# Kernel optimization log

Measured on AMD Instinct MI355X. Metric: run time of the kernel, lower is better.

## Reference

```python
import jax, jax.numpy as jnp
import numpy as np

T = 1 << 20  # hash-table size for bilateral-grid vertices
PRIMES = jnp.array([73856093, 19349663, 83492791, 49979687, 24036583], dtype=jnp.int32)
RGB2YUV = jnp.array([[0.299, 0.587, 0.114], [-0.168736, -0.331264, 0.5], [0.5, -0.418688, -0.081312]], dtype=jnp.float32)
YUV_OFF = jnp.array([0.0, 128.0, 128.0], dtype=jnp.float32)
SIG = jnp.array([8.0, 2.0, 2.0], dtype=jnp.float32)  # sigma_luma, sigma_chroma, sigma_chroma (mode=0)
SIGMA_SPATIAL = 7.0
LAM = 200.0
A_DIAG_MIN = 1e-5
CG_MAXITER = 12
BISTO_ITERS = 10
EPS = 1e-12
DIM = 5


def _hash(c):  # (..., 5) int32 -> flat bin id in [0, T)
    return (c * PRIMES).sum(-1) & (T - 1)


def _norm_max(x):
    s = jnp.clip(jnp.max(x, axis=(1, 2, 3), keepdims=True), 1e-5, 1.0)
    return x / s


def _conv(x, w, b, stride, pad):
    y = jax.lax.conv_general_dilated(x, w, (stride, stride), ((pad, pad), (pad, pad)), dimension_numbers=('NCHW', 'OIHW', 'NCHW'))
    return y + b[None, :, None, None]


def _gn(x, g, b, groups=2, eps=1e-5):
    B, C, H, W = x.shape
    xg = x.reshape(B, groups, -1)
    mu = xg.mean(-1, keepdims=True)
    var = xg.var(-1, keepdims=True)
    xg = (xg - mu) * jax.lax.rsqrt(var + eps)
    return xg.reshape(B, C, H, W) * g[None, :, None, None] + b[None, :, None, None]


def _reppad(x):
    return jnp.pad(x, ((0, 0), (0, 0), (1, 1), (1, 1)), mode='edge')


def _resize(x, h, w):
    B, C = x.shape[:2]
    return jax.image.resize(x, (B, C, h, w), method='linear')


def _bilateral_solve(guide_hwc, target_hwc, conf_hw):
    # fast bilateral solver (Barron & Poole): splat -> bistochastize -> PCG on grid -> slice
    H, W, C = target_hwc.shape
    N = H * W
    yuv = guide_hwc.reshape(N, 3) @ RGB2YUV.T + YUV_OFF
    yy, xx = jnp.meshgrid(jnp.arange(H, dtype=jnp.float32), jnp.arange(W, dtype=jnp.float32), indexing='ij')
    sp = jnp.stack([xx, yy], -1).reshape(N, 2) / SIGMA_SPATIAL
    coords = jnp.concatenate([jnp.floor(sp), jnp.floor(yuv / SIG)], -1).astype(jnp.int32)  # (N,5)
    h = _hash(coords)
    occ = jnp.zeros((T,), bool).at[h].set(True)
    ctab = jnp.full((T, 5), -1, jnp.int32).at[h].set(coords)
    # precompute 1-2-1 blur neighbor gathers along each of the 5 grid dims
    nhs, vals = [], []
    for d in range(DIM):
        for off in (-1, 1):
            nc = ctab.at[:, d].add(off)
            nh = _hash(nc)
            nhs.append(nh)
            vals.append(occ & occ[nh] & jnp.all(ctab[nh] == nc, axis=-1))
    occf = occ[:, None]

    def blur(v):  # (T,k)
        out = (2.0 * DIM) * v
        for nh, va in zip(nhs, vals):
            out = out + jnp.where(va[:, None], v[nh], 0.0)
        return jnp.where(occf, out, 0.0)

    def splat(v):  # (N,k) -> (T,k)
        return jax.ops.segment_sum(v, h, num_segments=T)

    # bistochastization
    m = splat(jnp.ones((N, 1), jnp.float32))
    n = occf.astype(jnp.float32)
    for _ in range(BISTO_ITERS):
        n = jnp.sqrt(n * m / (blur(n) + EPS))
    m = n * blur(n)

    w = conf_hw.reshape(N, 1)
    w_splat = splat(w)
    b = splat(w * target_hwc.reshape(N, C))
    y0 = b / (w_splat + EPS)
    A_diag = jnp.maximum(LAM * (m - (2.0 * DIM) * n * n) + w_splat, A_DIAG_MIN)
    Minv = 1.0 / A_diag

    def A(v):  # A = lam*(Dm - Dn B Dn) + diag(splat(w))
        return LAM * (m * v - n * blur(n * v)) + w_splat * v

    x0 = y0
    r0 = b - A(x0)
    z0 = Minv * r0

    def step(st, _):
        x, r, z, p = st
        Ap = A(p)
        rz = (r * z).sum(0)
        alpha = rz / ((p * Ap).sum(0) + EPS)
        x = x + alpha * p
        r = r - alpha * Ap
        z = Minv * r
        beta = (r * z).sum(0) / (rz + EPS)
        p = z + beta * p
        return (x, r, z, p), None

    (x, _, _, _), _ = jax.lax.scan(step, (x0, r0, z0, z0), None, length=CG_MAXITER)
    return x[h].reshape(H, W, C)  # slice


def _forward(image, feature, pred, w1, b1, g1, be1, w2, b2, g2, be2, wd1, bd1, gd1, bed1, wd2, bd2, gd2, bed2, wf, bf):
    image = _norm_max(image)
    feature = _norm_max(feature)
    inp = jax.lax.stop_gradient(jnp.concatenate([image, pred], axis=1))
    x1 = jax.nn.relu(_gn(_conv(_reppad(inp), w1, b1, 2, 0), g1, be1))
    x2 = jax.nn.relu(_gn(_conv(_reppad(x1), w2, b2, 2, 0), g2, be2))
    dx1 = jax.nn.relu(_gn(_conv(x2, wd1, bd1, 1, 1), gd1, bed1))
    dx1 = _resize(dx1, x1.shape[2], x1.shape[3])
    dx2 = jax.nn.relu(_gn(_conv(jnp.concatenate([dx1, x1], 1), wd2, bd2, 1, 1), gd2, bed2))
    dx2 = _resize(dx2, inp.shape[2], inp.shape[3])
    conf = 0.5 * (jnp.tanh(_conv(_reppad(dx2), wf, bf, 1, 0)) + 1.0)
    conf = conf / jnp.maximum(conf.max(), 1e-5)
    guide = jax.lax.stop_gradient(feature) * 255.0
    out = jax.vmap(_bilateral_solve)(guide.transpose(0, 2, 3, 1), pred.transpose(0, 2, 3, 1), conf[:, 0])
    return out.transpose(0, 3, 1, 2), conf


def setup_inputs():
    key = jax.random.key(0)
    ks = jax.random.split(key, 8)
    B, H, W = 2, 384, 512

    def cw(k, shape, fan_in):
        return jax.random.normal(k, shape, jnp.float32) * (1.0 / np.sqrt(fan_in))

    return {
        'image': jax.random.uniform(ks[0], (B, 3, H, W), jnp.float32),
        'feature': jax.random.uniform(ks[1], (B, 3, H, W), jnp.float32),
        'pred': jax.random.uniform(ks[2], (B, 3, H, W), jnp.float32),
        'w1': cw(ks[3], (16, 6, 4, 4), 6 * 16), 'b1': jnp.zeros((16,), jnp.float32),
        'g1': jnp.ones((16,), jnp.float32), 'be1': jnp.zeros((16,), jnp.float32),
        'w2': cw(ks[4], (16, 16, 4, 4), 16 * 16), 'b2': jnp.zeros((16,), jnp.float32),
        'g2': jnp.ones((16,), jnp.float32), 'be2': jnp.zeros((16,), jnp.float32),
        'wd1': cw(ks[5], (16, 16, 3, 3), 16 * 9), 'bd1': jnp.zeros((16,), jnp.float32),
        'gd1': jnp.ones((16,), jnp.float32), 'bed1': jnp.zeros((16,), jnp.float32),
        'wd2': cw(ks[6], (16, 32, 3, 3), 32 * 9), 'bd2': jnp.zeros((16,), jnp.float32),
        'gd2': jnp.ones((16,), jnp.float32), 'bed2': jnp.zeros((16,), jnp.float32),
        'wf': cw(ks[7], (1, 16, 3, 3), 16 * 9), 'bf': jnp.zeros((1,), jnp.float32),
    }


def reference(image, feature, pred, w1, b1, g1, be1, w2, b2, g2, be2, wd1, bd1, gd1, bed1, wd2, bd2, gd2, bed2, wf, bf):
    return _forward(image, feature, pred, w1, b1, g1, be1, w2, b2, g2, be2, wd1, bd1, gd1, bed1, wd2, bd2, gd2, bed2, wf, bf)
```

## Files before the change

### kernel.cpp

```cpp
#include <hip/hip_runtime.h>

#define H_ 384
#define W_ 512
#define N_ (H_*W_)
#define B_ 2
#define T_ 1048576
#define TMASK_ 0xFFFFFu
#define G2N_ ((2*N_)/256)
#define G2T_ ((2*T_)/256)
#define CHS_ 64
#define RZ0_ 192
#define RZB_ 2688
#define PAP0_ 5568
#define PAPB_ 2496
#define GN0_ 10560

__device__ __forceinline__ int prime(int d){
  switch(d){
    case 0: return 73856093;
    case 1: return 19349663;
    case 2: return 83492791;
    case 3: return 49979687;
    default: return 24036583;
  }
}

__device__ __forceinline__ float clampScale(float s){ return fminf(fmaxf(s,1e-5f),1.0f); }

__device__ __forceinline__ double blockReduceD(double v){
  __shared__ double sh[4];
  for(int s=32;s>0;s>>=1) v += __shfl_down(v,s,64);
  int lane=threadIdx.x&63, w=threadIdx.x>>6;
  if(lane==0) sh[w]=v;
  __syncthreads();
  double r = sh[0]+sh[1]+sh[2]+sh[3];
  __syncthreads();
  return r;
}
__device__ __forceinline__ float blockReduceMaxF(float v){
  __shared__ float sh[4];
  for(int s=32;s>0;s>>=1) v = fmaxf(v,__shfl_down(v,s,64));
  int lane=threadIdx.x&63, w=threadIdx.x>>6;
  if(lane==0) sh[w]=v;
  __syncthreads();
  float r = fmaxf(fmaxf(sh[0],sh[1]),fmaxf(sh[2],sh[3]));
  __syncthreads();
  return r;
}

__device__ __forceinline__ void redAdd(double* base, int c, double v){
  atomicAdd(&base[c*CHS_ + ((blockIdx.x&7)<<3)], v);
}
__device__ __forceinline__ float redSum(const double* base, int c){
  double s=0.0;
  #pragma unroll
  for(int j=0;j<8;j++) s += base[c*CHS_ + j*8];
  return (float)s;
}

__device__ __forceinline__ void gnStats(const double* acc, int b, int c, double len,
                                        float* mf, float* rs){
  const double* ba = acc + (b*2 + (c>>3))*128;
  double s=0.0,s2=0.0;
  #pragma unroll
  for(int j=0;j<8;j++){ s+=ba[j*8]; s2+=ba[64+j*8]; }
  double mean = s/len;
  double var = s2/len - mean*mean;
  *rs = (float)(1.0/sqrt(var + 1e-5));
  *mf = (float)mean;
}


__global__ __launch_bounds__(256) void k_maxes(const float4* img4, const float4* feat4, float* scal){
  const int PB = (3*N_)/4;
  for(int b=0;b<2;b++){
    float lm=0.f, lf=0.f;
    for(int idx = blockIdx.x*256+threadIdx.x; idx<PB; idx += gridDim.x*256){
      float4 a=img4[(size_t)b*PB+idx], c=feat4[(size_t)b*PB+idx];
      lm=fmaxf(lm, fmaxf(fmaxf(a.x,a.y),fmaxf(a.z,a.w)));
      lf=fmaxf(lf, fmaxf(fmaxf(c.x,c.y),fmaxf(c.z,c.w)));
    }
    lm=blockReduceMaxF(lm); lf=blockReduceMaxF(lf);
    if(threadIdx.x==0){
      atomicMax((int*)&scal[b],   __float_as_int(lm));
      atomicMax((int*)&scal[2+b], __float_as_int(lf));
    }
  }
}

template<int PLANE4>
__global__ __launch_bounds__(256) void k_gnrelu(const float4* in, float4* out, const double* acc,
                                                const float* gamma, const float* beta){
  int idx = blockIdx.x*256 + threadIdx.x;
  int t = idx / PLANE4;
  int c = t & 15, b = t >> 4;
  __shared__ float smf, srs, sg, sbe;
  if(threadIdx.x==0){
    float mf, rs;
    gnStats(acc, b, c, 8.0*(double)(PLANE4*4), &mf, &rs);
    smf=mf; srs=rs; sg=gamma[c]; sbe=beta[c];
  }
  __syncthreads();
  float mf=smf, rs=srs, g=sg, be=sbe;
  float4 v = in[idx];
  v.x = fmaxf((v.x-mf)*rs*g+be, 0.f);
  v.y = fmaxf((v.y-mf)*rs*g+be, 0.f);
  v.z = fmaxf((v.z-mf)*rs*g+be, 0.f);
  v.w = fmaxf((v.w-mf)*rs*g+be, 0.f);
  out[idx] = v;
}

template<bool SCALEA,int NCH,int K,int S,bool EDGE,int IH,int IW,int NOC>
__device__ __forceinline__ void conv_accum(const float* __restrict__ plane0, int icBase, float sA,
                                           int oy, int ox, const float* wlds, float acc[NOC]){
  for(int ic=0; ic<NCH; ic++){
    const float* plane = plane0 + (size_t)ic*IH*IW;
    #pragma unroll
    for(int ky=0;ky<K;ky++){
      int iy = oy*S + ky - 1;
      int cy = min(max(iy,0),IH-1);
      bool yin = (iy>=0)&&(iy<IH);
      const float* row = plane + cy*IW;
      #pragma unroll
      for(int kx=0;kx<K;kx++){
        int ix = ox*S + kx - 1;
        float v;
        if(EDGE){
          int cx = min(max(ix,0),IW-1);
          v = row[cx];
          if(SCALEA) v = v / sA;
        } else {
          bool inb = yin && ix>=0 && ix<IW;
          if(inb){
            v = row[ix];
            if(SCALEA) v = v / sA;
          } else v = 0.f;
        }
        const float* wp = &wlds[((icBase+ic)*K*K + ky*K + kx)*NOC];
        #pragma unroll
        for(int q=0;q<NOC;q++) acc[q] += v*wp[q];
      }
    }
  }
}

template<bool SCALEA,int ICA,int ICB,int K,int S,bool EDGE,int IH,int IW,int OH,int OW,int OCSPLIT>
__global__ __launch_bounds__(256) void k_convT(const float* __restrict__ inA, const float* __restrict__ inB,
                        const float* __restrict__ wt, const float* __restrict__ bias,
                        float* __restrict__ out, double* gnaccOut, const float* scal){
  constexpr int IC = ICA+ICB;
  constexpr int NOC = 16/OCSPLIT;
  constexpr int PB = (B_*OH*OW)/256;
  __shared__ float wlds[IC*K*K*NOC];
  __shared__ float blds[NOC];
  int pb  = blockIdx.x % PB;
  int ocg = blockIdx.x / PB;
  int ocBase = ocg*NOC;
  for(int i=threadIdx.x; i<IC*K*K*NOC; i+=256){
    int q = i % NOC, ickk = i / NOC;
    wlds[i] = wt[(ocBase+q)*IC*K*K + ickk];
  }
  if(threadIdx.x<NOC) blds[threadIdx.x]=bias[ocBase+threadIdx.x];
  __syncthreads();
  int idx = pb*256+threadIdx.x;
  int ox = idx % OW; int t=idx/OW; int oy=t%OH; int b=t/OH;
  float sA = SCALEA ? clampScale(scal[b]) : 1.0f;
  float acc[NOC];
  #pragma unroll
  for(int q=0;q<NOC;q++) acc[q]=0.f;
  conv_accum<SCALEA,ICA,K,S,EDGE,IH,IW,NOC>(inA + (size_t)b*ICA*IH*IW, 0, sA, oy, ox, wlds, acc);
  if constexpr(ICB>0)
    conv_accum<false,(ICB>0?ICB:1),K,S,EDGE,IH,IW,NOC>(inB + (size_t)b*ICB*IH*IW, ICA, 1.0f, oy, ox, wlds, acc);
  double s=0.0,s2=0.0;
  #pragma unroll
  for(int q=0;q<NOC;q++){
    float vv = acc[q] + blds[q];
    out[(((size_t)b*16+(ocBase+q))*OH+oy)*OW+ox] = vv;
    s += vv; s2 += (double)vv*(double)vv;
  }
  s=blockReduceD(s); s2=blockReduceD(s2);
  if(threadIdx.x==0){
    int grp = ocBase>>3;
    int sub = (blockIdx.x&7)<<3;
    atomicAdd(&gnaccOut[(b*2+grp)*128 + sub],      s);
    atomicAdd(&gnaccOut[(b*2+grp)*128 + 64 + sub], s2);
  }
}

template<int IH,int IW>
__global__ __launch_bounds__(256) void k_resize2x(const float* __restrict__ in, float* __restrict__ out,
                                                  const double* acc, const float* gamma, const float* beta){
  constexpr int QP = IH*IW;
  constexpr int OW = 2*IW;
  int idx = blockIdx.x*256 + threadIdx.x;
  int q = idx % QP; int t = idx / QP;
  int qx = q % IW, qy = q / IW;
  int c = t & 15, b = t >> 4;
  __shared__ float smf, srs, sg, sbe;
  if(threadIdx.x==0){
    float mf, rs;
    gnStats(acc, b, c, 8.0*(double)QP, &mf, &rs);
    smf=mf; srs=rs; sg=gamma[c]; sbe=beta[c];
  }
  __syncthreads();
  float mf=smf, rs=srs, g=sg, be=sbe;
  const float* plane = in + (size_t)t*QP;
  int ym = max(qy-1,0), yp = min(qy+1,IH-1);
  int xm = max(qx-1,0), xp = min(qx+1,IW-1);
  const float* r0 = plane + ym*IW;
  const float* r1 = plane + qy*IW;
// ... 10 lines not shown
  *(float2*)po        = rE;
  *(float2*)(po + OW) = rO;
}

__global__ __launch_bounds__(256) void k_conv5(const float* in, const float* wf, const float* bf,
                                               float* confr, float* scal){
  int idx = blockIdx.x*256 + threadIdx.x;
  int ph = idx % (N_/2); int b = idx / (N_/2);
  int oyh = ph / W_, ox = ph % W_;
  int oy0 = oyh*2;
  float acc0 = bf[0], acc1 = bf[0];
  for(int ic=0; ic<16; ic++){
    const float* plane = in + ((size_t)b*16+ic)*N_;
    #pragma unroll
    for(int ky=0;ky<3;ky++){
      int iy0 = min(max(oy0+ky-1,0),H_-1);
      int iy1 = min(max(oy0+ky,0),H_-1);
      const float* row0 = plane + iy0*W_;
      const float* row1 = plane + iy1*W_;
      #pragma unroll
      for(int kx=0;kx<3;kx++){
        int ix = min(max(ox+kx-1,0),W_-1);
        float w = wf[(ic*3+ky)*3+kx];
        acc0 += row0[ix]*w;
        acc1 += row1[ix]*w;
      }
    }
  }
  float c0 = 0.5f*(tanhf(acc0)+1.0f);
  float c1 = 0.5f*(tanhf(acc1)+1.0f);
  confr[(size_t)b*N_ + oy0*W_ + ox]     = c0;
  confr[(size_t)b*N_ + (oy0+1)*W_ + ox] = c1;
  float mx = blockReduceMaxF(fmaxf(c0,c1));
  if(threadIdx.x==0) atomicMax((int*)&scal[4], __float_as_int(mx));
}


__global__ __launch_bounds__(256) void k_px1(const float* feat, const float* scal,
                                             int* hpix, int2* cpix2, int* winner){
  int idx = blockIdx.x*256 + threadIdx.x;
  int b = idx / N_, pix = idx % N_;
  int y = pix / W_, x = pix % W_;
  float sF = clampScale(scal[2+b]);
  const float* fb = feat + (size_t)b*3*N_;
  float R  = __fmul_rn(__fdiv_rn(fb[pix],      sF), 255.0f);
  float G  = __fmul_rn(__fdiv_rn(fb[N_+pix],   sF), 255.0f);
  float Bl = __fmul_rn(__fdiv_rn(fb[2*N_+pix], sF), 255.0f);
  float Y = __fadd_rn(__fadd_rn(__fadd_rn(__fmul_rn(0.299f,R),     __fmul_rn(0.587f,G)),  __fmul_rn(0.114f,Bl)), 0.0f);
  float U = __fadd_rn(__fadd_rn(__fadd_rn(__fmul_rn(-0.168736f,R), __fmul_rn(-0.331264f,G)), __fmul_rn(0.5f,Bl)), 128.0f);
  float V = __fadd_rn(__fadd_rn(__fadd_rn(__fmul_rn(0.5f,R),       __fmul_rn(-0.418688f,G)), __fmul_rn(-0.081312f,Bl)), 128.0f);
  int c[5];
  c[0] = (int)floorf(__fdiv_rn((float)x, 7.0f));
  c[1] = (int)floorf(__fdiv_rn((float)y, 7.0f));
  c[2] = (int)floorf(__fdiv_rn(Y, 8.0f));
  c[3] = (int)floorf(__fdiv_rn(U, 2.0f));
  c[4] = (int)floorf(__fdiv_rn(V, 2.0f));
  unsigned hh = 0;
  #pragma unroll
  for(int d=0;d<5;d++) hh += (unsigned)c[d]*(unsigned)prime(d);
  hh &= TMASK_;
  hpix[idx]=(int)hh;
  cpix2[idx]=make_int2(c[0] | (c[1]<<10) | (c[2]<<20), c[3] | (c[4]<<10));
  atomicMax(&winner[(size_t)b*T_+(int)hh], pix);
}


__global__ __launch_bounds__(256) void k_cnt(const int* winner, int* bcnt){
  int t = blockIdx.x*256 + threadIdx.x;
  bool occ = winner[t] >= 0;
  __shared__ int wc[4];
  unsigned long long mk = __ballot(occ);
  int lane = threadIdx.x & 63, w = threadIdx.x >> 6;
  if(lane==0) wc[w] = __popcll(mk);
  __syncthreads();
  if(threadIdx.x==0) bcnt[blockIdx.x] = wc[0]+wc[1]+wc[2]+wc[3];
}

__global__ __launch_bounds__(256) void k_scan(const int* bcnt, int* boff, int* count){
  __shared__ int sh[256];
  __shared__ int carry;
  if(threadIdx.x==0) carry=0;
  __syncthreads();
  for(int chunk=0; chunk<32; ++chunk){
    if(chunk==16){
      if(threadIdx.x==0){ count[0]=carry; carry=0; }
      __syncthreads();
    }
    int v = bcnt[chunk*256+threadIdx.x];
    sh[threadIdx.x]=v;
    __syncthreads();
    for(int s2=1;s2<256;s2<<=1){
      int add = (threadIdx.x>=s2)? sh[threadIdx.x-s2] : 0;
      __syncthreads();
      sh[threadIdx.x]+=add;
      __syncthreads();
    }
    int incl = sh[threadIdx.x];
    boff[chunk*256+threadIdx.x] = carry + incl - v;
    __syncthreads();
    if(threadIdx.x==255) carry += incl;
    __syncthreads();
  }
  if(threadIdx.x==0) count[1]=carry;
}

__global__ __launch_bounds__(256) void k_cmp(const int* winner, const int* boff,
                                             int2* cidx2, int* slot_of){
  int t = blockIdx.x*256 + threadIdx.x;
  int b = t / T_;
  int wn = winner[t];
  bool occ = wn >= 0;
  __shared__ int wc[4];
  unsigned long long mk = __ballot(occ);
  int lane = threadIdx.x & 63, w = threadIdx.x >> 6;
  if(lane==0) wc[w] = __popcll(mk);
  __syncthreads();
  int wpre = 0;
  for(int k2=0;k2<4;k2++) if(k2<w) wpre += wc[k2];
  if(occ){
    int li = boff[blockIdx.x] + wpre + __popcll(mk & ((1ull<<lane)-1ull));
    int gi = b*N_ + li;
    cidx2[t] = make_int2(gi, wn);
    slot_of[gi] = t - b*T_;
  }
}

__global__ __launch_bounds__(256) void k_px3(int* hpix_gpix, const int2* cidx2, const float* confr,
                                             const float* scal, float* confout, const float* pred,
                                             float* mcomp, float4* splat4, float* mcompE, float* splatE){
  int idx = blockIdx.x*256 + threadIdx.x;
  int b = idx / N_, pix = idx % N_;
  int2 cw = cidx2[(size_t)b*T_ + hpix_gpix[idx]];
  int gi = cw.x;
  hpix_gpix[idx] = gi;
  float w = confr[idx] / fmaxf(scal[4], 1e-5f);
  confout[idx] = w;
  const float* pb = pred + (size_t)b*3*N_;
  float v0 = __fmul_rn(w, pb[pix]);
  float v1 = __fmul_rn(w, pb[N_+pix]);
  float v2 = __fmul_rn(w, pb[2*N_+pix]);
  if(cw.y == pix){
    splat4[gi] = make_float4(v0,v1,v2,w);
    mcomp[gi] = 1.0f;
  } else {
    float* s = splatE + 4*(size_t)gi;
    atomicAdd(s+0, v0);
    atomicAdd(s+1, v1);
    atomicAdd(s+2, v2);
    atomicAdd(s+3, w);
    atomicAdd(&mcompE[gi], 1.0f);
  }
}

__global__ __launch_bounds__(256) void k_bisto0(const int* count, const int* slot_of,
                      const int2* cpix2, const int2* cidx2, int* nbr,
                      float* mcomp, const float* mcompE, float4* splat4, const float4* splatE4,
                      float* nd){
  int i = blockIdx.x*256 + threadIdx.x;
  int b = i / N_, li = i - b*N_;
  if(li >= count[b]) return;
  int hh = slot_of[i];
  const int2* c2b = cidx2 + (size_t)b*T_;
  int2 cself = c2b[hh];
  int2 cp = cpix2[(size_t)b*N_ + cself.y];
  float4 sp = splat4[i]; float4 se = splatE4[i];
  sp.x+=se.x; sp.y+=se.y; sp.z+=se.z; sp.w+=se.w;
  splat4[i]=sp;
  float mTot = mcomp[i] + mcompE[i];
  mcomp[i]=mTot;
  float bv = 10.f;
  #pragma unroll
  for(int j=0;j<10;j++){
    int d=j>>1; int off=(j&1)?1:-1;
    unsigned nh = ((unsigned)hh + (unsigned)(off*prime(d))) & TMASK_;
    int nb = -1;
    int2 cn2 = c2b[nh];
    if(cn2.y>=0){
      int2 cn = cpix2[(size_t)b*N_ + cn2.y];
      int e0 = cp.x + (d==0?off: d==1?off*(1<<10) : d==2?off*(1<<20) : 0);
      int e1 = cp.y + (d==3?off: d==4?off*(1<<10) : 0);
      if(cn.x==e0 && cn.y==e1) nb = cn2.x;
    }
    nbr[(size_t)j*(2*N_)+i]=nb;
    if(nb>=0) bv += 1.0f;
  }
  nd[i] = sqrtf(1.0f*mTot/(bv+1e-12f));
}

__global__ __launch_bounds__(256) void k_bisto(const int* count, const int* nbr,
                                               const float* ns, float* nd, const float* mc){
  int i = blockIdx.x*256 + threadIdx.x;
  int b = i / N_, li = i - b*N_;
  if(li >= count[b]) return;
  float nv = ns[i];
  float bv = 10.f*nv;
  #pragma unroll
  for(int j=0;j<10;j++){
    int nb = nbr[(size_t)j*(2*N_)+i];
    if(nb>=0) bv += ns[nb];
  }
  nd[i] = sqrtf(nv*mc[i]/(bv+1e-12f));
}

__global__ __launch_bounds__(256) void k_Ar0(const int* count, const int* nbr, const float* n,
                      const float4* splat4, float4* meta4, float4* x4, float4* r4, float4* p4,
                      double* rz0){
  int i = blockIdx.x*256 + threadIdx.x;
  int b = i / N_, li = i - b*N_;
  double a0=0.0,a1=0.0,a2=0.0;
  if(li < count[b]){
    float4 vb4 = splat4[i];
    float wsi = vb4.w;
    float nv = n[i];
    float x0 = vb4.x/(wsi+1e-12f);
    float x1 = vb4.y/(wsi+1e-12f);
    float x2 = vb4.z/(wsi+1e-12f);
    float bv = 10.f*nv;
    float s0=10.f*(nv*x0), s1=10.f*(nv*x1), s2=10.f*(nv*x2);
    #pragma unroll
    for(int j=0;j<10;j++){
      int nb = nbr[(size_t)j*(2*N_)+i];
      if(nb>=0){
        float4 vbn = splat4[nb];
        float nn = n[nb];
        bv += nn;
        s0 += nn*(vbn.x/(vbn.w+1e-12f));
        s1 += nn*(vbn.y/(vbn.w+1e-12f));
        s2 += nn*(vbn.z/(vbn.w+1e-12f));
      }
    }
    float mfin = nv*bv;
    float Ad = fmaxf(200.0f*(mfin - 10.f*nv*nv) + wsi, 1e-5f);
    float mi = 1.0f/Ad;
    float A0 = 200.f*(mfin*x0 - nv*s0) + wsi*x0;
    float A1 = 200.f*(mfin*x1 - nv*s1) + wsi*x1;
    float A2 = 200.f*(mfin*x2 - nv*s2) + wsi*x2;
    float r0v = vb4.x-A0, r1v = vb4.y-A1, r2v = vb4.z-A2;
    float z0=mi*r0v, z1=mi*r1v, z2=mi*r2v;
    meta4[i]=make_float4(nv,mfin,wsi,mi);
    x4[i]=make_float4(x0,x1,x2,0.f);
    r4[i]=make_float4(r0v,r1v,r2v,mi);
    p4[i]=make_float4(z0,z1,z2,nv);
    a0=(double)r0v*z0; a1=(double)r1v*z1; a2=(double)r2v*z2;
  }
  a0=blockReduceD(a0); a1=blockReduceD(a1); a2=blockReduceD(a2);
  if(threadIdx.x==0){
    double* base = rz0 + b*RZB_;
    redAdd(base,0,a0); redAdd(base,1,a1); redAdd(base,2,a2);
  }
}

__global__ __launch_bounds__(256) void k_Ap(const int* count, const int* nbr, const float4* meta4,
                     const float4* r4, const float4* pOld4, float4* pNew4, float4* Ap4,
                     const double* bNum, const double* bDen, int bstr, double* pAp){
  int i = blockIdx.x*256 + threadIdx.x;
  int b = i / N_, li = i - b*N_;
  double a0=0.0,a1=0.0,a2=0.0;
  const double* nB_ = bNum + b*bstr;
  const double* dB_ = bDen + b*bstr;
  float be0 = redSum(nB_,0) / (redSum(dB_,0)+1e-12f);
  float be1 = redSum(nB_,1) / (redSum(dB_,1)+1e-12f);
  float be2 = redSum(nB_,2) / (redSum(dB_,2)+1e-12f);
  if(li < count[b]){
    float4 mt = meta4[i];
    float nv = mt.x, mfin = mt.y, wsi = mt.z;
    float4 rs = r4[i];
    float4 ps = pOld4[i];
    float p0 = rs.w*rs.x + be0*ps.x;
    float p1 = rs.w*rs.y + be1*ps.y;
    float p2 = rs.w*rs.z + be2*ps.z;
    float s0=10.f*(nv*p0), s1=10.f*(nv*p1), s2=10.f*(nv*p2);
    #pragma unroll
    for(int j=0;j<10;j++){
      int nb = nbr[(size_t)j*(2*N_)+i];
      if(nb>=0){
        float4 rn = r4[nb];
        float4 pn = pOld4[nb];
        float nn = pn.w;
        s0 += nn*(rn.w*rn.x + be0*pn.x);
        s1 += nn*(rn.w*rn.y + be1*pn.y);
        s2 += nn*(rn.w*rn.z + be2*pn.z);
      }
    }
    float A0 = 200.f*(mfin*p0 - nv*s0) + wsi*p0;
    float A1 = 200.f*(mfin*p1 - nv*s1) + wsi*p1;
    float A2 = 200.f*(mfin*p2 - nv*s2) + wsi*p2;
    pNew4[i]=make_float4(p0,p1,p2,nv);
    Ap4[i]=make_float4(A0,A1,A2,0.f);
    a0=(double)p0*A0; a1=(double)p1*A1; a2=(double)p2*A2;
  }
  a0=blockReduceD(a0); a1=blockReduceD(a1); a2=blockReduceD(a2);
  if(threadIdx.x==0){
    double* base = pAp + b*PAPB_;
    redAdd(base,0,a0); redAdd(base,1,a1); redAdd(base,2,a2);
  }
}

__global__ __launch_bounds__(256) void k_upd1(const int* count, float4* x4, float4* r4,
                       const float4* p4, const float4* Ap4,
                       const double* rzCur, const double* pApC, double* rzNew, int doRz){
  int i = blockIdx.x*256 + threadIdx.x;
  int b = i / N_, li = i - b*N_;
  double a0=0.0,a1=0.0,a2=0.0;
  const double* rc = rzCur + b*RZB_;
  const double* pc = pApC  + b*PAPB_;
  float al0 = redSum(rc,0) / (redSum(pc,0)+1e-12f);
  float al1 = redSum(rc,1) / (redSum(pc,1)+1e-12f);
  float al2 = redSum(rc,2) / (redSum(pc,2)+1e-12f);
  if(li < count[b]){
    float4 xv = x4[i];
    float4 rv = r4[i];
    float4 pv = p4[i];
    float4 av = Ap4[i];
    float mi = rv.w;
    float x0=xv.x+al0*pv.x, x1=xv.y+al1*pv.y, x2=xv.z+al2*pv.z;
    float r0v=rv.x-al0*av.x, r1v=rv.y-al1*av.y, r2v=rv.z-al2*av.z;
    float z0=mi*r0v, z1=mi*r1v, z2=mi*r2v;
    x4[i]=make_float4(x0,x1,x2,0.f);
    r4[i]=make_float4(r0v,r1v,r2v,mi);
    a0=(double)r0v*z0; a1=(double)r1v*z1; a2=(double)r2v*z2;
  }
  if(doRz){
    a0=blockReduceD(a0); a1=blockReduceD(a1); a2=blockReduceD(a2);
    if(threadIdx.x==0){
      double* base = rzNew + b*RZB_;
      redAdd(base,0,a0); redAdd(base,1,a1); redAdd(base,2,a2);
    }
  }
}

__global__ __launch_bounds__(256) void k_out(const float4* x4, const int* gpix, float* out){
  int idx = blockIdx.x*256 + threadIdx.x;
  int b = idx / N_, pix = idx % N_;
  float4 xv = x4[gpix[idx]];
  out[((size_t)(b*3+0))*N_+pix] = xv.x;
  out[((size_t)(b*3+1))*N_+pix] = xv.y;
  out[((size_t)(b*3+2))*N_+pix] = xv.z;
}


extern "C" void kernel_launch(void* const* d_in, const int* in_sizes, int n_in,
                              void* d_out, int out_size, void* d_ws, size_t ws_size,
                              hipStream_t stream){
  const float* image=(const float*)d_in[0];
  const float* feature=(const float*)d_in[1];
  const float* pred=(const float*)d_in[2];
  const float* w1=(const float*)d_in[3];  const float* b1=(const float*)d_in[4];
  const float* g1=(const float*)d_in[5];  const float* be1=(const float*)d_in[6];
  const float* w2=(const float*)d_in[7];  const float* b2=(const float*)d_in[8];
  const float* g2=(const float*)d_in[9];  const float* be2=(const float*)d_in[10];
  const float* wd1=(const float*)d_in[11];const float* bd1=(const float*)d_in[12];
  const float* gd1=(const float*)d_in[13];const float* bed1=(const float*)d_in[14];
  const float* wd2=(const float*)d_in[15];const float* bd2=(const float*)d_in[16];
  const float* gd2=(const float*)d_in[17];const float* bed2=(const float*)d_in[18];
  const float* wf=(const float*)d_in[19]; const float* bf=(const float*)d_in[20];
  float* outp=(float*)d_out;
  float* confout = outp + (size_t)B_*3*N_;

  char* wsb=(char*)d_ws;
  float* scal=(float*)wsb;
  int* count=(int*)(wsb+256);
  double* scalD=(double*)(wsb+4096);
  double* zeroD = scalD;
  auto rzArr  = [&](int it)->double*{ return scalD + RZ0_  + it*192; };
  auto pApArr = [&](int it)->double*{ return scalD + PAP0_ + it*192; };
  auto gnAcc  = [&](int L)->double*{ return scalD + GN0_ + L*512; };

  size_t off = 131072;
  auto alloc=[&](size_t bytes)->char*{ char* pp=wsb+off; off=(off+bytes+255)&~(size_t)255; return pp; };
  const size_t ALLOC0 = off;

  float* x1   =(float*)alloc((size_t)B_*16*192*256*4);
  float* x1n  =(float*)alloc((size_t)B_*16*192*256*4);
  float* x2   =(float*)alloc((size_t)B_*16*96*128*4);
  float* x2n  =(float*)alloc((size_t)B_*16*96*128*4);
  float* dx1  =(float*)alloc((size_t)B_*16*96*128*4);
  float* dx1r =(float*)alloc((size_t)B_*16*192*256*4);
  float* dx2  =(float*)alloc((size_t)B_*16*192*256*4);
  float* dx2r =(float*)alloc((size_t)B_*16*N_*4);

  off = ALLOC0;
  int*    winner =(int*)   alloc((size_t)2*T_*4);
  int2*   cidx2  =(int2*)  alloc((size_t)2*T_*8);
  int*    hpix   =(int*)   alloc((size_t)2*N_*4);
  int2*   cpix2  =(int2*)  alloc((size_t)2*N_*8);
  int*    slot_of=(int*)   alloc((size_t)2*N_*4);
  int*    nbr    =(int*)   alloc((size_t)2*N_*10*4);
  float*  mcomp  =(float*) alloc((size_t)2*N_*4);
  float4* splat4 =(float4*)alloc((size_t)2*N_*16);
  float*  mcompE =(float*) alloc((size_t)2*N_*4);
  float*  splatE =(float*) alloc((size_t)2*N_*16);
  float*  nA     =(float*) alloc((size_t)2*N_*4);
  float*  nB     =(float*) alloc((size_t)2*N_*4);
  float4* meta4  =(float4*)alloc((size_t)2*N_*16);
  float4* x4     =(float4*)alloc((size_t)2*N_*16);
  float4* r4     =(float4*)alloc((size_t)2*N_*16);
  float4* pA4    =(float4*)alloc((size_t)2*N_*16);
  float4* pB4    =(float4*)alloc((size_t)2*N_*16);
  int*    bcnt   =(int*)   alloc((size_t)G2T_*4);
  int*    boff   =(int*)   alloc((size_t)G2T_*4);
  float4* Ap4    = splat4;
  float*  confr  = (float*)pB4;

  dim3 blk(256);

  hipMemsetAsync(wsb, 0, 4096 + 12608*8, stream);

  k_maxes<<<128,blk,0,stream>>>((const float4*)image,(const float4*)feature,scal);

  k_convT<true,3,3,4,2,true,384,512,192,256,2><<<2*((B_*192*256)/256),blk,0,stream>>>(
      image,pred,w1,b1,x1,gnAcc(0),scal);
  k_gnrelu<12288><<<(B_*16*12288)/256,blk,0,stream>>>((const float4*)x1,(float4*)x1n,gnAcc(0),g1,be1);
  k_convT<false,16,0,4,2,true,192,256,96,128,8><<<8*((B_*96*128)/256),blk,0,stream>>>(
      x1n,x1n,w2,b2,x2,gnAcc(1),scal);
  k_gnrelu<3072><<<(B_*16*3072)/256,blk,0,stream>>>((const float4*)x2,(float4*)x2n,gnAcc(1),g2,be2);
  k_convT<false,16,0,3,1,false,96,128,96,128,8><<<8*((B_*96*128)/256),blk,0,stream>>>(
      x2n,x2n,wd1,bd1,dx1,gnAcc(2),scal);
  k_resize2x<96,128><<<(B_*16*96*128)/256,blk,0,stream>>>(dx1, dx1r, gnAcc(2), gd1, bed1);
  k_convT<false,16,16,3,1,false,192,256,192,256,2><<<2*((B_*192*256)/256),blk,0,stream>>>(
      dx1r,x1n,wd2,bd2,dx2,gnAcc(3),scal);
  k_resize2x<192,256><<<(B_*16*192*256)/256,blk,0,stream>>>(dx2, dx2r, gnAcc(3), gd2, bed2);

  k_conv5<<<(B_*(N_/2))/256,blk,0,stream>>>(dx2r, wf, bf, confr, scal);

  hipMemsetAsync(winner, 0xFF, (size_t)2*T_*4, stream);
  hipMemsetAsync(cidx2,  0xFF, (size_t)2*T_*8, stream);
  hipMemsetAsync(mcomp,  0,    (size_t)2*N_*40, stream);
  k_px1<<<G2N_,blk,0,stream>>>(feature,scal,hpix,cpix2,winner);
  k_cnt<<<G2T_,blk,0,stream>>>(winner,bcnt);
  k_scan<<<1,blk,0,stream>>>(bcnt,boff,count);
  k_cmp<<<G2T_,blk,0,stream>>>(winner,boff,cidx2,slot_of);
  k_px3<<<G2N_,blk,0,stream>>>(hpix,cidx2,confr,scal,confout,pred,mcomp,splat4,mcompE,splatE);

  k_bisto0<<<G2N_,blk,0,stream>>>(count,slot_of,cpix2,cidx2,nbr,mcomp,mcompE,splat4,(const float4*)splatE,nA);
  for(int it=1; it<10; ++it){
    float* src = (it&1) ? nA : nB;
    float* dst = (it&1) ? nB : nA;
    k_bisto<<<G2N_,blk,0,stream>>>(count,nbr,src,dst,mcomp);
  }
  float* nfin = nB;

  k_Ar0<<<G2N_,blk,0,stream>>>(count,nbr,nfin,splat4,meta4,x4,r4,pA4,rzArr(0));

  float4* pbuf[2]={pA4,pB4};
  for(int it=0; it<12; ++it){
    const double* bN = (it==0) ? zeroD : rzArr(it);
    const double* bD = (it==0) ? zeroD : rzArr(it-1);
    int bstr = (it==0) ? 0 : RZB_;
    k_Ap<<<G2N_,blk,0,stream>>>(count,nbr,meta4,r4,pbuf[it&1],pbuf[(it+1)&1],Ap4,bN,bD,bstr,pApArr(it));
    k_upd1<<<G2N_,blk,0,stream>>>(count,x4,r4,pbuf[(it+1)&1],Ap4,rzArr(it),pApArr(it),rzArr(it+1),(it<11)?1:0);
  }
  k_out<<<G2N_,blk,0,stream>>>(x4,hpix,outp);

  (void)in_sizes; (void)n_in; (void)out_size; (void)ws_size;
}
```

Before: 771.9 us.

## Fuse bistochastization and PCG solver into one persistent cooperative kernel

```diff
diff --git a/kernel.cpp b/kernel.cpp
--- a/kernel.cpp
+++ b/kernel.cpp
@@ -1,4 +1,7 @@
 #include <hip/hip_runtime.h>
+#include <hip/hip_cooperative_groups.h>
+
+namespace cg = cooperative_groups;
 
 #define H_ 384
 #define W_ 512
@@ -56,6 +59,13 @@
   #pragma unroll
   for(int j=0;j<8;j++) s += base[c*CHS_ + j*8];
   return (float)s;
+}
+__device__ __forceinline__ double redSumAtomic(const double* base, int c){
+  double s=0.0;
+  #pragma unroll
+  for(int j=0;j<8;j++)
+    s += __hip_atomic_load(&base[c*CHS_ + j*8], __ATOMIC_RELAXED, __HIP_MEMORY_SCOPE_AGENT);
+  return s;
 }
 
 __device__ __forceinline__ void gnStats(const double* acc, int b, int c, double len,
@@ -372,6 +382,301 @@
   }
 }
 
+template<int K>
+__global__ __launch_bounds__(256, (K==1?3:2)) void k_solver(
+    const int* __restrict__ count, const int* __restrict__ slot_of,
+    const int2* __restrict__ cpix2, const int2* __restrict__ cidx2,
+    int* __restrict__ nbr, const float* __restrict__ mcomp,
+    const float* __restrict__ mcompE, float4* __restrict__ splat4,
+    const float4* __restrict__ splatE4, float* __restrict__ nA,
+    float* __restrict__ nB, float4* __restrict__ r4,
+    float4* __restrict__ pA4, float4* __restrict__ pB4,
+    float4* __restrict__ x4, double* __restrict__ scalD,
+    const int* __restrict__ gpix, float* __restrict__ outp){
+  constexpr int STRIDE = N_/K;
+  cg::grid_group gg = cg::this_grid();
+  int tid = blockIdx.x*256 + threadIdx.x;
+  int cnt0 = count[0], cnt1 = count[1];
+  bool lv_[2][K];
+  float mt_[2][K], nv_[2][K];
+  #pragma unroll
+  for(int e=0;e<2;e++)
+    #pragma unroll
+    for(int k=0;k<K;k++)
+      lv_[e][k] = (tid + k*STRIDE) < (e ? cnt1 : cnt0);
+
+  #pragma unroll
+  for(int e=0;e<2;e++){
+    #pragma unroll
+    for(int k=0;k<K;k++){
+      if(lv_[e][k]){
+        int i = tid + k*STRIDE + e*N_;
+        int hh = slot_of[i];
+        const int2* c2b = cidx2 + (size_t)e*T_;
+        int2 cself = c2b[hh];
+        int2 cp = cpix2[(size_t)e*N_ + cself.y];
+        float4 sp = splat4[i]; float4 se = splatE4[i];
+        sp.x+=se.x; sp.y+=se.y; sp.z+=se.z; sp.w+=se.w;
+        splat4[i]=sp;
+        float mTot = mcomp[i] + mcompE[i];
+        mt_[e][k]=mTot;
+        float bv = 10.f;
+        #pragma unroll
+        for(int j=0;j<10;j++){
+          int d=j>>1; int off=(j&1)?1:-1;
+          unsigned nh = ((unsigned)hh + (unsigned)(off*prime(d))) & TMASK_;
+          int nb = -1;
+          int2 cn2 = c2b[nh];
+          if(cn2.y>=0){
+            int2 cn = cpix2[(size_t)e*N_ + cn2.y];
+            int e0 = cp.x + (d==0?off: d==1?off*(1<<10) : d==2?off*(1<<20) : 0);
+            int e1 = cp.y + (d==3?off: d==4?off*(1<<10) : 0);
+            if(cn.x==e0 && cn.y==e1) nb = cn2.x;
+          }
+          nbr[(size_t)j*(2*N_)+i]=nb;
+          if(nb>=0) bv += 1.0f;
+        }
+        float nd0 = sqrtf(1.0f*mTot/(bv+1e-12f));
+        nv_[e][k]=nd0;
+        nA[i]=nd0;
+      }
+    }
+  }
+  gg.sync();
+
+  const float* nsrc = nA; float* ndst = nB;
+  for(int it=1; it<10; ++it){
+    #pragma unroll
+    for(int e=0;e<2;e++){
+      #pragma unroll
+      for(int k=0;k<K;k++){
+        if(lv_[e][k]){
+          int i = tid + k*STRIDE + e*N_;
+          float nvs = nv_[e][k];
+          float bv = 10.f*nvs;
+          #pragma unroll
+          for(int j=0;j<10;j++){
+            int nb = nbr[(size_t)j*(2*N_)+i];
+            if(nb>=0) bv += nsrc[nb];
+          }
+          float nn = sqrtf(nvs*mt_[e][k]/(bv+1e-12f));
+          nv_[e][k]=nn;
+          ndst[i]=nn;
+        }
+      }
+    }
+    gg.sync();
+    float* ts = (float*)nsrc; nsrc = ndst; ndst = ts;
+  }
+
+  float xx_[2][K][3], rr_[2][K][3], pp_[2][K][3], Ap_[2][K][3];
+  float mi_[2][K], mfin_[2][K], wsi_[2][K];
+  {
+    double acc[2][3] = {{0.0,0.0,0.0},{0.0,0.0,0.0}};
+    #pragma unroll
+    for(int e=0;e<2;e++){
+      #pragma unroll
+      for(int k=0;k<K;k++){
+        if(lv_[e][k]){
+          int i = tid + k*STRIDE + e*N_;
+          float4 vb4 = splat4[i];
+          float wsi = vb4.w;
+          float nv = nv_[e][k];
+          float x0 = vb4.x/(wsi+1e-12f);
+          float x1 = vb4.y/(wsi+1e-12f);
+          float x2 = vb4.z/(wsi+1e-12f);
+          float bv = 10.f*nv;
+          float s0=10.f*(nv*x0), s1=10.f*(nv*x1), s2=10.f*(nv*x2);
+          #pragma unroll
+          for(int j=0;j<10;j++){
+            int nb = nbr[(size_t)j*(2*N_)+i];
+            if(nb>=0){
+              float4 vbn = splat4[nb];
+              float nn = nsrc[nb];
+              bv += nn;
+              s0 += nn*(vbn.x/(vbn.w+1e-12f));
+              s1 += nn*(vbn.y/(vbn.w+1e-12f));
+              s2 += nn*(vbn.z/(vbn.w+1e-12f));
+            }
+          }
+          float mfin = nv*bv;
+          float Ad = fmaxf(200.0f*(mfin - 10.f*nv*nv) + wsi, 1e-5f);
+          float mi = 1.0f/Ad;
+          float A0 = 200.f*(mfin*x0 - nv*s0) + wsi*x0;
+          float A1 = 200.f*(mfin*x1 - nv*s1) + wsi*x1;
+          float A2 = 200.f*(mfin*x2 - nv*s2) + wsi*x2;
+          float r0v = vb4.x-A0, r1v = vb4.y-A1, r2v = vb4.z-A2;
+          float z0=mi*r0v, z1=mi*r1v, z2=mi*r2v;
+          r4[i]=make_float4(r0v,r1v,r2v,mi);
+          pA4[i]=make_float4(z0,z1,z2,nv);
+          xx_[e][k][0]=x0; xx_[e][k][1]=x1; xx_[e][k][2]=x2;
+          rr_[e][k][0]=r0v; rr_[e][k][1]=r1v; rr_[e][k][2]=r2v;
+          pp_[e][k][0]=z0; pp_[e][k][1]=z1; pp_[e][k][2]=z2;
+          mi_[e][k]=mi; mfin_[e][k]=mfin; wsi_[e][k]=wsi;
+          acc[e][0]+=(double)r0v*z0; acc[e][1]+=(double)r1v*z1; acc[e][2]+=(double)r2v*z2;
+        }
+      }
+    }
+    #pragma unroll
+    for(int e=0;e<2;e++){
+      #pragma unroll
+      for(int c=0;c<3;c++){
+        double r = blockReduceD(acc[e][c]);
+        if(threadIdx.x==0)
+          atomicAdd(&scalD[RZ0_ + e*RZB_ + c*CHS_ + ((blockIdx.x&7)<<3)], r);
+      }
+    }
+  }
+  gg.sync();
+
+  for(int it=0; it<12; ++it){
+    __shared__ float sbe[2][3];
+    if(threadIdx.x==0){
+      #pragma unroll
+      for(int b=0;b<2;b++){
+        if(it==0){ sbe[b][0]=0.f; sbe[b][1]=0.f; sbe[b][2]=0.f; }
+        else{
+          const double* nB_ = scalD + RZ0_ + it*192     + b*RZB_;
+          const double* dB_ = scalD + RZ0_ + (it-1)*192 + b*RZB_;
+          #pragma unroll
+          for(int c=0;c<3;c++){
+            float num = (float)redSumAtomic(nB_,c);
+            float den = (float)redSumAtomic(dB_,c);
+            sbe[b][c] = num / (den + 1e-12f);
+          }
+        }
+      }
+    }
+    __syncthreads();
+    const float4* pOld = (it&1)? pB4 : pA4;
+    float4*       pNew = (it&1)? pA4 : pB4;
+    double acc[2][3] = {{0.0,0.0,0.0},{0.0,0.0,0.0}};
+    #pragma unroll
+    for(int e=0;e<2;e++){
+      #pragma unroll
+      for(int k=0;k<K;k++){
+        if(lv_[e][k]){
+          int i = tid + k*STRIDE + e*N_;
+          float be0=sbe[e][0], be1=sbe[e][1], be2=sbe[e][2];
+          float mi=mi_[e][k], mfin=mfin_[e][k], wsi=wsi_[e][k];
+          float nvv = nv_[e][k];
+          float p0 = mi*rr_[e][k][0] + be0*pp_[e][k][0];
+          float p1 = mi*rr_[e][k][1] + be1*pp_[e][k][1];
+          float p2 = mi*rr_[e][k][2] + be2*pp_[e][k][2];
+          float s0=10.f*(nvv*p0), s1=10.f*(nvv*p1), s2=10.f*(nvv*p2);
+          #pragma unroll
+          for(int j=0;j<10;j++){
+            int nb = nbr[(size_t)j*(2*N_)+i];
+            if(nb>=0){
+              float4 rn = r4[nb];
+              float4 pn = pOld[nb];
+              float nn = pn.w;
+              s0 += nn*(rn.w*rn.x + be0*pn.x);
+              s1 += nn*(rn.w*rn.y + be1*pn.y);
+              s2 += nn*(rn.w*rn.z + be2*pn.z);
+            }
+          }
+          float A0 = 200.f*(mfin*p0 - nvv*s0) + wsi*p0;
+          float A1 = 200.f*(mfin*p1 - nvv*s1) + wsi*p1;
+          float A2 = 200.f*(mfin*p2 - nvv*s2) + wsi*p2;
+          pNew[i]=make_float4(p0,p1,p2,nvv);
+          pp_[e][k][0]=p0; pp_[e][k][1]=p1; pp_[e][k][2]=p2;
+          Ap_[e][k][0]=A0; Ap_[e][k][1]=A1; Ap_[e][k][2]=A2;
+          acc[e][0]+=(double)p0*A0; acc[e][1]+=(double)p1*A1; acc[e][2]+=(double)p2*A2;
+        }
+      }
+    }
+    #pragma unroll
+    for(int e=0;e<2;e++){
+      #pragma unroll
+      for(int c=0;c<3;c++){
+        double r = blockReduceD(acc[e][c]);
+        if(threadIdx.x==0)
+          atomicAdd(&scalD[PAP0_ + it*192 + e*PAPB_ + c*CHS_ + ((blockIdx.x&7)<<3)], r);
+      }
+    }
+    gg.sync();
+
+    __shared__ float sal[2][3];
+    if(threadIdx.x==0){
+      #pragma unroll
+      for(int b=0;b<2;b++){
+        const double* rc = scalD + RZ0_  + it*192 + b*RZB_;
+        const double* pc = scalD + PAP0_ + it*192 + b*PAPB_;
+        #pragma unroll
+        for(int c=0;c<3;c++){
+          float num = (float)redSumAtomic(rc,c);
+          float den = (float)redSumAtomic(pc,c);
+          sal[b][c] = num / (den + 1e-12f);
+        }
+      }
+    }
+    __syncthreads();
+    double bacc[2][3] = {{0.0,0.0,0.0},{0.0,0.0,0.0}};
+    #pragma unroll
+    for(int e=0;e<2;e++){
+      #pragma unroll
+      for(int k=0;k<K;k++){
+        if(lv_[e][k]){
+          int i = tid + k*STRIDE + e*N_;
+          float al0=sal[e][0], al1=sal[e][1], al2=sal[e][2];
+          xx_[e][k][0] += al0*pp_[e][k][0];
+          xx_[e][k][1] += al1*pp_[e][k][1];
+          xx_[e][k][2] += al2*pp_[e][k][2];
+          if(it<11){
+            float r0v = rr_[e][k][0] - al0*Ap_[e][k][0];
+            float r1v = rr_[e][k][1] - al1*Ap_[e][k][1];
+            float r2v = rr_[e][k][2] - al2*Ap_[e][k][2];
+            rr_[e][k][0]=r0v; rr_[e][k][1]=r1v; rr_[e][k][2]=r2v;
+            float mi = mi_[e][k];
+            r4[i]=make_float4(r0v,r1v,r2v,mi);
+            bacc[e][0]+=(double)r0v*(mi*r0v);
+            bacc[e][1]+=(double)r1v*(mi*r1v);
+            bacc[e][2]+=(double)r2v*(mi*r2v);
+          }
+        }
+      }
+    }
+    if(it<11){
+      #pragma unroll
+      for(int e=0;e<2;e++){
+        #pragma unroll
+        for(int c=0;c<3;c++){
+          double r = blockReduceD(bacc[e][c]);
+          if(threadIdx.x==0)
+            atomicAdd(&scalD[RZ0_ + (it+1)*192 + e*RZB_ + c*CHS_ + ((blockIdx.x&7)<<3)], r);
+        }
+      }
+    }
+    gg.sync();
+  }
+
+  #pragma unroll
+  for(int e=0;e<2;e++){
+    #pragma unroll
+    for(int k=0;k<K;k++){
+      if(lv_[e][k]){
+        int i = tid + k*STRIDE + e*N_;
+        x4[i]=make_float4(xx_[e][k][0],xx_[e][k][1],xx_[e][k][2],0.f);
+      }
+    }
+  }
+  gg.sync();
+  #pragma unroll
+  for(int e=0;e<2;e++){
+    #pragma unroll
+    for(int k=0;k<K;k++){
+      int pix = tid + k*STRIDE;
+      int i = pix + e*N_;
+      float4 xv = x4[gpix[i]];
+      outp[((size_t)(e*3+0))*N_+pix] = xv.x;
+      outp[((size_t)(e*3+1))*N_+pix] = xv.y;
+      outp[((size_t)(e*3+2))*N_+pix] = xv.z;
+    }
+  }
+}
+
+
 __global__ __launch_bounds__(256) void k_bisto0(const int* count, const int* slot_of,
                       const int2* cpix2, const int2* cidx2, int* nbr,
                       float* mcomp, const float* mcompE, float4* splat4, const float4* splatE4,
@@ -652,25 +957,55 @@
   k_cmp<<<G2T_,blk,0,stream>>>(winner,boff,cidx2,slot_of);
   k_px3<<<G2N_,blk,0,stream>>>(hpix,cidx2,confr,scal,confout,pred,mcomp,splat4,mcompE,splatE);
 
-  k_bisto0<<<G2N_,blk,0,stream>>>(count,slot_of,cpix2,cidx2,nbr,mcomp,mcompE,splat4,(const float4*)splatE,nA);
-  for(int it=1; it<10; ++it){
-    float* src = (it&1) ? nA : nB;
-    float* dst = (it&1) ? nB : nA;
-    k_bisto<<<G2N_,blk,0,stream>>>(count,nbr,src,dst,mcomp);
-  }
-  float* nfin = nB;
-
-  k_Ar0<<<G2N_,blk,0,stream>>>(count,nbr,nfin,splat4,meta4,x4,r4,pA4,rzArr(0));
-
-  float4* pbuf[2]={pA4,pB4};
-  for(int it=0; it<12; ++it){
-    const double* bN = (it==0) ? zeroD : rzArr(it);
-    const double* bD = (it==0) ? zeroD : rzArr(it-1);
-    int bstr = (it==0) ? 0 : RZB_;
-    k_Ap<<<G2N_,blk,0,stream>>>(count,nbr,meta4,r4,pbuf[it&1],pbuf[(it+1)&1],Ap4,bN,bD,bstr,pApArr(it));
-    k_upd1<<<G2N_,blk,0,stream>>>(count,x4,r4,pbuf[(it+1)&1],Ap4,rzArr(it),pApArr(it),rzArr(it+1),(it<11)?1:0);
-  }
-  k_out<<<G2N_,blk,0,stream>>>(x4,hpix,outp);
+  bool done = false;
+  {
+    const int* countc = count;
+    const int* slotc  = slot_of;
+    const int2* cpix2c = cpix2;
+    const int2* cidx2c = cidx2;
+    const float* mcompc = mcomp;
+    const float* mcompEc = mcompE;
+    const float4* splatE4c = (const float4*)splatE;
+    const int* gpixc = hpix;
+    void* kargs[] = {
+      (void*)&countc, (void*)&slotc, (void*)&cpix2c, (void*)&cidx2c,
+      (void*)&nbr, (void*)&mcompc, (void*)&mcompEc, (void*)&splat4,
+      (void*)&splatE4c, (void*)&nA, (void*)&nB, (void*)&r4,
+      (void*)&pA4, (void*)&pB4, (void*)&x4, (void*)&scalD,
+      (void*)&gpixc, (void*)&outp };
+    int occ1=0, occ2=0;
+    hipOccupancyMaxActiveBlocksPerMultiprocessor(&occ1,
+        reinterpret_cast<const void*>(&k_solver<1>), 256, 0);
+    hipOccupancyMaxActiveBlocksPerMultiprocessor(&occ2,
+        reinterpret_cast<const void*>(&k_solver<2>), 256, 0);
+    if(occ1 >= 3){
+      done = (hipSuccess == hipLaunchCooperativeKernel(
+          reinterpret_cast<const void*>(&k_solver<1>), dim3(N_/256), blk, kargs, 0, stream));
+    }
+    if(!done && occ2 >= 2){
+      done = (hipSuccess == hipLaunchCooperativeKernel(
+          reinterpret_cast<const void*>(&k_solver<2>), dim3(N_/512), blk, kargs, 0, stream));
+    }
+  }
+  if(!done){
+    k_bisto0<<<G2N_,blk,0,stream>>>(count,slot_of,cpix2,cidx2,nbr,mcomp,mcompE,splat4,(const float4*)splatE,nA);
+    for(int it=1; it<10; ++it){
+      float* src = (it&1) ? nA : nB;
+      float* dst = (it&1) ? nB : nA;
+      k_bisto<<<G2N_,blk,0,stream>>>(count,nbr,src,dst,mcomp);
+    }
+    float* nfin = nB;
+    k_Ar0<<<G2N_,blk,0,stream>>>(count,nbr,nfin,splat4,meta4,x4,r4,pA4,rzArr(0));
+    float4* pbuf[2]={pA4,pB4};
+    for(int it=0; it<12; ++it){
+      const double* bN = (it==0) ? zeroD : rzArr(it);
+      const double* bD = (it==0) ? zeroD : rzArr(it-1);
+      int bstr = (it==0) ? 0 : RZB_;
+      k_Ap<<<G2N_,blk,0,stream>>>(count,nbr,meta4,r4,pbuf[it&1],pbuf[(it+1)&1],Ap4,bN,bD,bstr,pApArr(it));
+      k_upd1<<<G2N_,blk,0,stream>>>(count,x4,r4,pbuf[(it+1)&1],Ap4,rzArr(it),pApArr(it),rzArr(it+1),(it<11)?1:0);
+    }
+    k_out<<<G2N_,blk,0,stream>>>(x4,hpix,outp);
+  }
 
   (void)in_sizes; (void)n_in; (void)out_size; (void)ws_size;
 }
```

After: 773.9 us. No clear change (+0.3%).

## Interleave preconditioned residual and direction in one CG buffer, hoist scalar reductions

Applied to the files above, without the earlier changes.

```diff
diff --git a/kernel.cpp b/kernel.cpp
--- a/kernel.cpp
+++ b/kernel.cpp
@@ -372,6 +372,7 @@
   }
 }
 
+
 __global__ __launch_bounds__(256) void k_bisto0(const int* count, const int* slot_of,
                       const int2* cpix2, const int2* cidx2, int* nbr,
                       float* mcomp, const float* mcompE, float4* splat4, const float4* splatE4,
@@ -423,7 +424,7 @@
 }
 
 __global__ __launch_bounds__(256) void k_Ar0(const int* count, const int* nbr, const float* n,
-                      const float4* splat4, float4* meta4, float4* x4, float4* r4, float4* p4,
+                      const float4* splat4, float4* meta4, float4* x4, float4* rS, float4* zp0,
                       double* rz0){
   int i = blockIdx.x*256 + threadIdx.x;
   int b = i / N_, li = i - b*N_;
@@ -459,8 +460,9 @@
     float z0=mi*r0v, z1=mi*r1v, z2=mi*r2v;
     meta4[i]=make_float4(nv,mfin,wsi,mi);
     x4[i]=make_float4(x0,x1,x2,0.f);
-    r4[i]=make_float4(r0v,r1v,r2v,mi);
-    p4[i]=make_float4(z0,z1,z2,nv);
+    rS[i]=make_float4(r0v,r1v,r2v,mi);
+    zp0[2*(size_t)i]   = make_float4(z0,z1,z2,mi);
+    zp0[2*(size_t)i+1] = make_float4(z0,z1,z2,nv);
     a0=(double)r0v*z0; a1=(double)r1v*z1; a2=(double)r2v*z2;
   }
   a0=blockReduceD(a0); a1=blockReduceD(a1); a2=blockReduceD(a2);
@@ -471,41 +473,49 @@
 }
 
 __global__ __launch_bounds__(256) void k_Ap(const int* count, const int* nbr, const float4* meta4,
-                     const float4* r4, const float4* pOld4, float4* pNew4, float4* Ap4,
+                     const float4* __restrict__ zpCur, float4* __restrict__ zpNext, float4* Ap4,
                      const double* bNum, const double* bDen, int bstr, double* pAp){
   int i = blockIdx.x*256 + threadIdx.x;
-  int b = i / N_, li = i - b*N_;
+  int b = (blockIdx.x*256) / N_;
+  int li = i - b*N_;
+  __shared__ float sbe[3];
+  if(threadIdx.x==0){
+    if(bstr==0){ sbe[0]=0.f; sbe[1]=0.f; sbe[2]=0.f; }
+    else{
+      const double* nB_ = bNum + b*bstr;
+      const double* dB_ = bDen + b*bstr;
+      #pragma unroll
+      for(int c=0;c<3;c++) sbe[c] = redSum(nB_,c) / (redSum(dB_,c)+1e-12f);
+    }
+  }
+  __syncthreads();
+  float be0=sbe[0], be1=sbe[1], be2=sbe[2];
   double a0=0.0,a1=0.0,a2=0.0;
-  const double* nB_ = bNum + b*bstr;
-  const double* dB_ = bDen + b*bstr;
-  float be0 = redSum(nB_,0) / (redSum(dB_,0)+1e-12f);
-  float be1 = redSum(nB_,1) / (redSum(dB_,1)+1e-12f);
-  float be2 = redSum(nB_,2) / (redSum(dB_,2)+1e-12f);
   if(li < count[b]){
     float4 mt = meta4[i];
     float nv = mt.x, mfin = mt.y, wsi = mt.z;
-    float4 rs = r4[i];
-    float4 ps = pOld4[i];
-    float p0 = rs.w*rs.x + be0*ps.x;
-    float p1 = rs.w*rs.y + be1*ps.y;
-    float p2 = rs.w*rs.z + be2*ps.z;
+    float4 zs = zpCur[2*(size_t)i];
+    float4 ps = zpCur[2*(size_t)i+1];
+    float p0 = zs.x + be0*ps.x;
+    float p1 = zs.y + be1*ps.y;
+    float p2 = zs.z + be2*ps.z;
     float s0=10.f*(nv*p0), s1=10.f*(nv*p1), s2=10.f*(nv*p2);
     #pragma unroll
     for(int j=0;j<10;j++){
       int nb = nbr[(size_t)j*(2*N_)+i];
       if(nb>=0){
-        float4 rn = r4[nb];
-        float4 pn = pOld4[nb];
+        float4 zn = zpCur[2*(size_t)nb];
+        float4 pn = zpCur[2*(size_t)nb+1];
         float nn = pn.w;
-        s0 += nn*(rn.w*rn.x + be0*pn.x);
-        s1 += nn*(rn.w*rn.y + be1*pn.y);
-        s2 += nn*(rn.w*rn.z + be2*pn.z);
+        s0 += nn*(zn.x + be0*pn.x);
+        s1 += nn*(zn.y + be1*pn.y);
+        s2 += nn*(zn.z + be2*pn.z);
       }
     }
     float A0 = 200.f*(mfin*p0 - nv*s0) + wsi*p0;
     float A1 = 200.f*(mfin*p1 - nv*s1) + wsi*p1;
     float A2 = 200.f*(mfin*p2 - nv*s2) + wsi*p2;
-    pNew4[i]=make_float4(p0,p1,p2,nv);
+    zpNext[2*(size_t)i+1]=make_float4(p0,p1,p2,nv);
     Ap4[i]=make_float4(A0,A1,A2,0.f);
     a0=(double)p0*A0; a1=(double)p1*A1; a2=(double)p2*A2;
   }
@@ -516,28 +526,35 @@
   }
 }
 
-__global__ __launch_bounds__(256) void k_upd1(const int* count, float4* x4, float4* r4,
-                       const float4* p4, const float4* Ap4,
+__global__ __launch_bounds__(256) void k_upd1(const int* count, float4* x4, float4* rS,
+                       const float4* __restrict__ zpNext_p, float4* __restrict__ zpNext_z,
+                       const float4* Ap4,
                        const double* rzCur, const double* pApC, double* rzNew, int doRz){
   int i = blockIdx.x*256 + threadIdx.x;
-  int b = i / N_, li = i - b*N_;
+  int b = (blockIdx.x*256) / N_;
+  int li = i - b*N_;
+  __shared__ float sal[3];
+  if(threadIdx.x==0){
+    const double* rc = rzCur + b*RZB_;
+    const double* pc = pApC  + b*PAPB_;
+    #pragma unroll
+    for(int c=0;c<3;c++) sal[c] = redSum(rc,c) / (redSum(pc,c)+1e-12f);
+  }
+  __syncthreads();
+  float al0=sal[0], al1=sal[1], al2=sal[2];
   double a0=0.0,a1=0.0,a2=0.0;
-  const double* rc = rzCur + b*RZB_;
-  const double* pc = pApC  + b*PAPB_;
-  float al0 = redSum(rc,0) / (redSum(pc,0)+1e-12f);
-  float al1 = redSum(rc,1) / (redSum(pc,1)+1e-12f);
-  float al2 = redSum(rc,2) / (redSum(pc,2)+1e-12f);
   if(li < count[b]){
     float4 xv = x4[i];
-    float4 rv = r4[i];
-    float4 pv = p4[i];
+    float4 rv = rS[i];
+    float4 pv = zpNext_p[2*(size_t)i+1];
     float4 av = Ap4[i];
     float mi = rv.w;
     float x0=xv.x+al0*pv.x, x1=xv.y+al1*pv.y, x2=xv.z+al2*pv.z;
     float r0v=rv.x-al0*av.x, r1v=rv.y-al1*av.y, r2v=rv.z-al2*av.z;
     float z0=mi*r0v, z1=mi*r1v, z2=mi*r2v;
     x4[i]=make_float4(x0,x1,x2,0.f);
-    r4[i]=make_float4(r0v,r1v,r2v,mi);
+    rS[i]=make_float4(r0v,r1v,r2v,mi);
+    zpNext_z[2*(size_t)i]=make_float4(z0,z1,z2,mi);
     a0=(double)r0v*z0; a1=(double)r1v*z1; a2=(double)r2v*z2;
   }
   if(doRz){
@@ -614,13 +631,13 @@
   float*  nB     =(float*) alloc((size_t)2*N_*4);
   float4* meta4  =(float4*)alloc((size_t)2*N_*16);
   float4* x4     =(float4*)alloc((size_t)2*N_*16);
-  float4* r4     =(float4*)alloc((size_t)2*N_*16);
-  float4* pA4    =(float4*)alloc((size_t)2*N_*16);
-  float4* pB4    =(float4*)alloc((size_t)2*N_*16);
+  float4* rS     =(float4*)alloc((size_t)2*N_*16);
+  float4* zpA4   =(float4*)alloc((size_t)2*N_*32);
+  float4* zpB4   =(float4*)alloc((size_t)2*N_*32);
   int*    bcnt   =(int*)   alloc((size_t)G2T_*4);
   int*    boff   =(int*)   alloc((size_t)G2T_*4);
   float4* Ap4    = splat4;
-  float*  confr  = (float*)pB4;
+  float*  confr  = (float*)zpB4;
 
   dim3 blk(256);
 
@@ -628,7 +645,7 @@
 
   k_maxes<<<128,blk,0,stream>>>((const float4*)image,(const float4*)feature,scal);
 
-  k_convT<true,3,3,4,2,true,384,512,192,256,2><<<2*((B_*192*256)/256),blk,0,stream>>>(
+  k_convT<true,3,3,4,2,true,384,512,192,256,4><<<4*((B_*192*256)/256),blk,0,stream>>>(
       image,pred,w1,b1,x1,gnAcc(0),scal);
   k_gnrelu<12288><<<(B_*16*12288)/256,blk,0,stream>>>((const float4*)x1,(float4*)x1n,gnAcc(0),g1,be1);
   k_convT<false,16,0,4,2,true,192,256,96,128,8><<<8*((B_*96*128)/256),blk,0,stream>>>(
@@ -637,7 +654,7 @@
   k_convT<false,16,0,3,1,false,96,128,96,128,8><<<8*((B_*96*128)/256),blk,0,stream>>>(
       x2n,x2n,wd1,bd1,dx1,gnAcc(2),scal);
   k_resize2x<96,128><<<(B_*16*96*128)/256,blk,0,stream>>>(dx1, dx1r, gnAcc(2), gd1, bed1);
-  k_convT<false,16,16,3,1,false,192,256,192,256,2><<<2*((B_*192*256)/256),blk,0,stream>>>(
+  k_convT<false,16,16,3,1,false,192,256,192,256,4><<<4*((B_*192*256)/256),blk,0,stream>>>(
       dx1r,x1n,wd2,bd2,dx2,gnAcc(3),scal);
   k_resize2x<192,256><<<(B_*16*192*256)/256,blk,0,stream>>>(dx2, dx2r, gnAcc(3), gd2, bed2);
 
@@ -660,15 +677,17 @@
   }
   float* nfin = nB;
 
-  k_Ar0<<<G2N_,blk,0,stream>>>(count,nbr,nfin,splat4,meta4,x4,r4,pA4,rzArr(0));
-
-  float4* pbuf[2]={pA4,pB4};
+  k_Ar0<<<G2N_,blk,0,stream>>>(count,nbr,nfin,splat4,meta4,x4,rS,zpA4,rzArr(0));
+
+  float4* zp[2]={zpA4,zpB4};
   for(int it=0; it<12; ++it){
+    float4* zpCur  = zp[it&1];
+    float4* zpNext = zp[(it+1)&1];
     const double* bN = (it==0) ? zeroD : rzArr(it);
     const double* bD = (it==0) ? zeroD : rzArr(it-1);
     int bstr = (it==0) ? 0 : RZB_;
-    k_Ap<<<G2N_,blk,0,stream>>>(count,nbr,meta4,r4,pbuf[it&1],pbuf[(it+1)&1],Ap4,bN,bD,bstr,pApArr(it));
-    k_upd1<<<G2N_,blk,0,stream>>>(count,x4,r4,pbuf[(it+1)&1],Ap4,rzArr(it),pApArr(it),rzArr(it+1),(it<11)?1:0);
+    k_Ap<<<G2N_,blk,0,stream>>>(count,nbr,meta4,zpCur,zpNext,Ap4,bN,bD,bstr,pApArr(it));
+    k_upd1<<<G2N_,blk,0,stream>>>(count,x4,rS,zpNext,zpNext,Ap4,rzArr(it),pApArr(it),rzArr(it+1),(it<11)?1:0);
   }
   k_out<<<G2N_,blk,0,stream>>>(x4,hpix,outp);
 
```

Measured after the change: 751.8 us. 1.03x faster.
